# Kernel optimization log

Hardware: AMD Instinct MI355X
Metric: run time of the kernel (lower is better)

## Reference

```python
import jax, jax.numpy as jnp
import numpy as np

NUM_HEADS = 8
HEAD_SIZE = 64
INPUT = 512
OUT = NUM_HEADS * HEAD_SIZE
B, S = 4, 2048


def setup_inputs() -> dict:
    key = jax.random.key(0)
    ks = jax.random.split(key, 6)
    return {
        "key": jax.random.normal(ks[0], (B, S, INPUT), dtype=jnp.float32),
        "key_mask": jnp.zeros((B, 1, 1, S), dtype=jnp.float32),
        "query": jax.random.normal(ks[1], (B, S, INPUT), dtype=jnp.float32),
        "value": jax.random.normal(ks[2], (B, S, INPUT), dtype=jnp.float32),
        "wq": jax.random.normal(ks[3], (INPUT, OUT), dtype=jnp.float32) * (INPUT ** -0.5),
        "wk": jax.random.normal(ks[4], (INPUT, OUT), dtype=jnp.float32) * (INPUT ** -0.5),
        "wv": jax.random.normal(ks[5], (INPUT, OUT), dtype=jnp.float32) * (INPUT ** -0.5),
    }


def _split_heads(x):
    # [B, S, H*hd] -> [B, H, S, hd]
    b, s, _ = x.shape
    return x.reshape(b, s, NUM_HEADS, HEAD_SIZE).transpose(0, 2, 1, 3)


def reference(key, key_mask, query, value, wq, wk, wv):
    q = _split_heads(query @ wq)   # [B,H,S,hd]
    k = _split_heads(key @ wk)
    v = _split_heads(value @ wv)
    scale = 1.0 / jnp.sqrt(jnp.asarray(HEAD_SIZE, q.dtype))
    logits = jnp.einsum('bhqd,bhkd->bhqk', q, k) * scale + key_mask
    attn = jax.nn.softmax(logits, axis=-1)
    out = jnp.einsum('bhqk,bhkd->bhqd', attn, v)  # [B,H,S,hd]
    out = out.transpose(0, 2, 1, 3).reshape(out.shape[0], out.shape[2], OUT)
    return out
```

## Files before the change

kernel.cpp:

```cpp
#include <hip/hip_runtime.h>

typedef _Float16 f16;
typedef f16 f16x8 __attribute__((ext_vector_type(8)));
typedef f16 f16x4 __attribute__((ext_vector_type(4)));
typedef f16 f16x2 __attribute__((ext_vector_type(2)));
typedef float f32x4 __attribute__((ext_vector_type(4)));
typedef unsigned int u32;

#define MFMA16(a, b, c) __builtin_amdgcn_mfma_f32_16x16x32_f16(a, b, c, 0, 0, 0)

#define BATCH 4
#define NHEADS 8
#define HDIM 64
#define SEQ 2048
#define DIN 512
#define DOUT 512
#define LOG2E 1.44269504f
#define C1 0.18033688f

__device__ __forceinline__ void gl_lds16(const void* g, const void* l) {
  __builtin_amdgcn_global_load_lds(
      (const __attribute__((address_space(1))) u32*)g,
      (__attribute__((address_space(3))) u32*)l, 16, 0, 0);
}

__device__ __forceinline__ float fexp2(float x) {
  float r;
  asm("v_exp_f32 %0, %1" : "=v"(r) : "v"(x));
  return r;
}

__device__ __forceinline__ f16x2 pk2(float a, float b) {
  return __builtin_bit_cast(f16x2, __builtin_amdgcn_cvt_pkrtz(a, b));
}

__device__ __forceinline__ f16x4 pk4(float a, float b, float c, float d) {
  f16x2 u0 = pk2(a, b), u1 = pk2(c, d);
  f16x4 r;
  r[0] = u0[0]; r[1] = u0[1]; r[2] = u1[0]; r[3] = u1[1];
  return r;
}

__global__ __launch_bounds__(256) void prep_w(
    const float* __restrict__ wq, const float* __restrict__ wk,
    const float* __restrict__ wv, f16* __restrict__ wT) {
  __shared__ float tile[64][65];
  const float* w = blockIdx.z == 0 ? wq : (blockIdx.z == 1 ? wk : wv);
  f16* out = wT + (size_t)blockIdx.z * DIN * DOUT;
  int k0 = blockIdx.x * 64, n0 = blockIdx.y * 64;
  int t = threadIdx.x;
  int c = t & 63, rb = t >> 6;
#pragma unroll
  for (int ph = 0; ph < 16; ++ph) {
    int r = ph * 4 + rb;
    tile[r][c] = w[(size_t)(k0 + r) * DOUT + n0 + c];
  }
  __syncthreads();
#pragma unroll
  for (int ph = 0; ph < 16; ++ph) {
    int n = ph * 4 + rb;
    out[(size_t)(n0 + n) * DIN + k0 + c] = (f16)tile[c][n];
  }
}

__global__ __launch_bounds__(256, 3) void qkv_gemm(
    const float* __restrict__ xq, const float* __restrict__ xk,
    const float* __restrict__ xv, const f16* __restrict__ wT,
    f16* __restrict__ Qo, f16* __restrict__ Ko, f16* __restrict__ Vt) {
  __shared__ __attribute__((aligned(16))) f16 smem[16384];
  f16* As = smem;
  f16* Bs = smem + 8192;
  f16* CT = smem;

  int gemm = blockIdx.z;
  const float* x = gemm == 0 ? xq : (gemm == 1 ? xk : xv);
  const f16* wt = wT + (size_t)gemm * DIN * DOUT;
  int bx = blockIdx.x;
  int m0 = (bx & 63) * 128, n0 = (bx >> 6) * 128;
  int t = threadIdx.x, w = t >> 6, lane = t & 63;
  int lr = lane & 15, lq = lane >> 4;
  int wm = (w >> 1) * 64, wn = (w & 1) * 64;

  int tr = t >> 4, tc = t & 15;
  const float* xg = x + (size_t)(m0 + tr) * DIN + tc * 4;
  int aw[8];
#pragma unroll
  for (int ph = 0; ph < 8; ++ph) {
    int r = tr + 16 * ph;
    int phys = (tc >> 1) ^ (r & 7);
    aw[ph] = r * 64 + phys * 8 + (tc & 1) * 4;
  }

  int srow = lane >> 3;
  int schunk = (lane & 7) ^ srow;
  const f16* gb[4];
  const f16* lbb[4];
#pragma unroll
  for (int j = 0; j < 4; ++j) {
    int br = w * 32 + j * 8;
    gb[j] = wt + (size_t)(n0 + br + srow) * DIN + schunk * 8;
    lbb[j] = &Bs[__builtin_amdgcn_readfirstlane(br * 64)];
  }
  int xo0 = ((0 * 4 + lq) ^ (lr & 7)) * 8;
  int xo1 = ((1 * 4 + lq) ^ (lr & 7)) * 8;

  f32x4 zero = {0.f, 0.f, 0.f, 0.f};
  f32x4 acc[4][4];
#pragma unroll
  for (int i = 0; i < 4; ++i)
#pragma unroll
    for (int j = 0; j < 4; ++j) acc[i][j] = zero;

  for (int k0 = 0; k0 < DIN; k0 += 64) {
    __syncthreads();
#pragma unroll
    for (int j = 0; j < 4; ++j) gl_lds16(gb[j] + k0, lbb[j]);
#pragma unroll
    for (int ph = 0; ph < 8; ++ph) {
      float4 a = *(const float4*)(xg + (size_t)ph * 16 * DIN + k0);
      *(f16x4*)&As[aw[ph]] = pk4(a.x, a.y, a.z, a.w);
    }
    __syncthreads();
#pragma unroll
    for (int c = 0; c < 2; ++c) {
      int xo = c ? xo1 : xo0;
      f16x8 xf[4], wf[4];
#pragma unroll
      for (int i = 0; i < 4; ++i)
        xf[i] = *(const f16x8*)&As[(wm + i * 16 + lr) * 64 + xo];
#pragma unroll
      for (int i = 0; i < 4; ++i)
        wf[i] = *(const f16x8*)&Bs[(wn + i * 16 + lr) * 64 + xo];
      if (gemm == 2) {
#pragma unroll
        for (int i = 0; i < 4; ++i)
#pragma unroll
          for (int j = 0; j < 4; ++j)
            acc[i][j] = MFMA16(xf[i], wf[j], acc[i][j]);
      } else {
#pragma unroll
        for (int i = 0; i < 4; ++i)
#pragma unroll
          for (int j = 0; j < 4; ++j)
            acc[i][j] = MFMA16(wf[i], xf[j], acc[i][j]);
      }
    }
  }

  __syncthreads();
  int b_ = m0 >> 11;
  int sl = m0 & 2047;

  if (gemm == 2) {
#pragma unroll
    for (int i = 0; i < 4; ++i) {
#pragma unroll
      for (int j = 0; j < 4; ++j) {
        int d = wn + j * 16 + lr;
        int lc = (wm >> 3) + i * 2 + (lq >> 1);
        int phys = lc ^ lr;
        *(f16x4*)&CT[d * 128 + phys * 8 + (lq & 1) * 4] =
            pk4(acc[i][j][0], acc[i][j][1], acc[i][j][2], acc[i][j][3]);
      }
    }
    __syncthreads();
    int tid16 = t & 15;
#pragma unroll
    for (int ph = 0; ph < 8; ++ph) {
      int d = ph * 16 + (t >> 4);
      int phys = tid16 ^ (d & 15);
      f16x8 vv = *(const f16x8*)&CT[d * 128 + phys * 8];
      int hgl = (n0 + d) >> 6, dd = (n0 + d) & 63;
      *(f16x8*)&Vt[(((size_t)b_ * NHEADS + hgl) * HDIM + dd) * SEQ + sl +
                   tid16 * 8] = vv;
    }
  } else {
    f16* O = gemm == 0 ? Qo : Ko;
    float sc = gemm == 0 ? C1 : 1.0f;
#pragma unroll
    for (int i = 0; i < 4; ++i) {
#pragma unroll
      for (int j = 0; j < 4; ++j) {
        int s = wm + j * 16 + lr;
        int lc = (wn >> 3) + i * 2 + (lq >> 1);
        int phys = lc ^ lr;
        *(f16x4*)&CT[s * 128 + phys * 8 + (lq & 1) * 4] =
            pk4(acc[i][j][0] * sc, acc[i][j][1] * sc, acc[i][j][2] * sc,
                acc[i][j][3] * sc);
      }
    }
    __syncthreads();
    int tid8 = t & 7;
    int hh = (t >> 3) & 1;
#pragma unroll
    for (int ph = 0; ph < 8; ++ph) {
      int s = ph * 16 + (t >> 4);
      int lc = hh * 8 + tid8;
      int phys = lc ^ (s & 15);
      f16x8 vv = *(const f16x8*)&CT[s * 128 + phys * 8];
      int hgl = (n0 >> 6) + hh;
      *(f16x8*)&O[(((size_t)b_ * NHEADS + hgl) * SEQ + sl + s) * HDIM +
                  tid8 * 8] = vv;
    }
  }
}

__global__ __launch_bounds__(256, 2) void flash_attn(
    const f16* __restrict__ Q, const f16* __restrict__ K,
    const f16* __restrict__ Vt, const float* __restrict__ mask,
    float* __restrict__ out) {
  __shared__ __attribute__((aligned(16))) f16 Ks[128 * 64];
  __shared__ __attribute__((aligned(16))) f16 Vs[64 * 128];
  __shared__ __attribute__((aligned(16))) f16 Ps[128 * 136];

  int bh = blockIdx.x, q0 = blockIdx.y * 128;
  int b = bh >> 3, h = bh & 7;
  int t = threadIdx.x, w = t >> 6, lane = t & 63;
  int lr = lane & 15, lq = lane >> 4;

  const f16* Qg = Q + (size_t)bh * SEQ * HDIM;
  const f16* Kg = K + (size_t)bh * SEQ * HDIM;
  const f16* Vg = Vt + (size_t)bh * HDIM * SEQ;
  const float* mg = mask + (size_t)b * SEQ;

  f16x8 qf[2][2];
#pragma unroll
  for (int u = 0; u < 2; ++u)
#pragma unroll
    for (int c = 0; c < 2; ++c)
      qf[u][c] = *(const f16x8*)(Qg +
                                 (size_t)(q0 + w * 32 + u * 16 + lr) * HDIM +
                                 c * 32 + lq * 8);

  int krow = lane >> 3;
  int kchunk = (lane & 7) ^ krow;
  const f16* gk[4];
  const f16* gv[4];
  const f16* lk[4];
  const f16* lv[4];
#pragma unroll
  for (int j = 0; j < 4; ++j) {
    int kbr = w * 32 + j * 8;
    gk[j] = Kg + (size_t)(kbr + krow) * HDIM + kchunk * 8;
    lk[j] = &Ks[__builtin_amdgcn_readfirstlane(kbr * 64)];
    int vbr = w * 16 + j * 4;
    int vchunk = (lane & 15) ^ (j * 4 + lq);
    gv[j] = Vg + (size_t)(vbr + lq) * SEQ + vchunk * 8;
    lv[j] = &Vs[__builtin_amdgcn_readfirstlane(vbr * 128)];
  }
  int xk0 = ((0 * 4 + lq) ^ (lr & 7)) * 8;
  int xk1 = ((1 * 4 + lq) ^ (lr & 7)) * 8;

  f32x4 zero = {0.f, 0.f, 0.f, 0.f};
  f32x4 acc[2][4];
#pragma unroll
  for (int u = 0; u < 2; ++u)
#pragma unroll
    for (int i = 0; i < 4; ++i) acc[u][i] = zero;
  float lsum[2] = {0.f, 0.f};

  for (int k0 = 0; k0 < SEQ; k0 += 128) {
    __syncthreads();
#pragma unroll
    for (int j = 0; j < 4; ++j) {
      gl_lds16(gk[j] + (size_t)k0 * HDIM, lk[j]);
      gl_lds16(gv[j] + k0, lv[j]);
    }
    __syncthreads();

    f32x4 s[2][8];
#pragma unroll
    for (int nt = 0; nt < 8; ++nt) {
      f16x8 kf0 = *(const f16x8*)&Ks[(nt * 16 + lr) * 64 + xk0];
      f16x8 kf1 = *(const f16x8*)&Ks[(nt * 16 + lr) * 64 + xk1];
      s[0][nt] = MFMA16(kf0, qf[0][0], zero);
      s[0][nt] = MFMA16(kf1, qf[0][1], s[0][nt]);
      s[1][nt] = MFMA16(kf0, qf[1][0], zero);
      s[1][nt] = MFMA16(kf1, qf[1][1], s[1][nt]);
    }

#pragma unroll
    for (int nt = 0; nt < 8; ++nt) {
      float4 mk = *(const float4*)(mg + k0 + nt * 16 + lq * 4);
#pragma unroll
      for (int u = 0; u < 2; ++u) {
        float p0 = fexp2(fmaf(mk.x, LOG2E, s[u][nt][0]));
        float p1 = fexp2(fmaf(mk.y, LOG2E, s[u][nt][1]));
        float p2 = fexp2(fmaf(mk.z, LOG2E, s[u][nt][2]));
        float p3 = fexp2(fmaf(mk.w, LOG2E, s[u][nt][3]));
        lsum[u] += (p0 + p1) + (p2 + p3);
        *(f16x4*)&Ps[(w * 32 + u * 16 + lr) * 136 + nt * 16 + lq * 4] =
            pk4(p0, p1, p2, p3);
      }
    }

#pragma unroll
    for (int ks = 0; ks < 4; ++ks) {
      f16x8 ap0 = *(const f16x8*)&Ps[(w * 32 + lr) * 136 + ks * 32 + lq * 8];
      f16x8 ap1 =
          *(const f16x8*)&Ps[(w * 32 + 16 + lr) * 136 + ks * 32 + lq * 8];
#pragma unroll
      for (int dt = 0; dt < 4; ++dt) {
        f16x8 bv = *(const f16x8*)&Vs[(dt * 16 + lr) * 128 +
                                      (((ks * 4 + lq) ^ lr) * 8)];
        acc[0][dt] = MFMA16(ap0, bv, acc[0][dt]);
        acc[1][dt] = MFMA16(ap1, bv, acc[1][dt]);
      }
    }
  }

#pragma unroll
  for (int u = 0; u < 2; ++u) {
    float l = lsum[u];
    l += __shfl_xor(l, 16);
    l += __shfl_xor(l, 32);
    float inv = 1.f / l;
    float iv[4];
#pragma unroll
    for (int r = 0; r < 4; ++r) iv[r] = __shfl(inv, lq * 4 + r);
#pragma unroll
    for (int dt = 0; dt < 4; ++dt) {
#pragma unroll
      for (int r = 0; r < 4; ++r) {
        int q = q0 + w * 32 + u * 16 + lq * 4 + r;
        int d = h * HDIM + dt * 16 + lr;
        out[((size_t)b * SEQ + q) * DOUT + d] = acc[u][dt][r] * iv[r];
      }
    }
  }
}

extern "C" void kernel_launch(void* const* d_in, const int* in_sizes, int n_in,
                              void* d_out, int out_size, void* d_ws,
                              size_t ws_size, hipStream_t stream) {
  const float* key = (const float*)d_in[0];
  const float* key_mask = (const float*)d_in[1];
  const float* query = (const float*)d_in[2];
  const float* value = (const float*)d_in[3];
  const float* wq = (const float*)d_in[4];
  const float* wk = (const float*)d_in[5];
  const float* wv = (const float*)d_in[6];
  float* out = (float*)d_out;

  char* ws = (char*)d_ws;
  f16* Qws = (f16*)(ws);
  f16* Kws = (f16*)(ws + 8388608);
  f16* Vtws = (f16*)(ws + 16777216);
  f16* wT = (f16*)(ws + 25165824);

  prep_w<<<dim3(8, 8, 3), 256, 0, stream>>>(wq, wk, wv, wT);
  qkv_gemm<<<dim3(256, 1, 3), 256, 0, stream>>>(query, key, value, wT, Qws,
                                                Kws, Vtws);
  flash_attn<<<dim3(32, 16), 256, 0, stream>>>(Qws, Kws, Vtws, key_mask, out);
}
```

Baseline: 183.8 us.

## Double-buffer K/V tiles with 64-key blocks and raise occupancy to three blocks

The attention loop now processes 64 keys per iteration instead of 128. K and V tiles are double-buffered in LDS, so the next tile's global-to-LDS load is issued before computing on the current one. The P buffer shrinks to a 64-wide XOR-swizzled layout instead of padding, which lowers LDS use enough to request three blocks per CU. This aims to overlap memory latency with MFMA work and raise occupancy. In exchange it adds twice as many loop iterations and barriers, and it relies on a single barrier per iteration to order the buffer reuse and the P writes and reads.

Result: slower. 195.6 us (+6.4%).

```diff
diff --git a/kernel.cpp b/kernel.cpp
--- a/kernel.cpp
+++ b/kernel.cpp
@@ -205,13 +205,13 @@
   }
 }
 
-__global__ __launch_bounds__(256, 2) void flash_attn(
+__global__ __launch_bounds__(256, 3) void flash_attn(
     const f16* __restrict__ Q, const f16* __restrict__ K,
     const f16* __restrict__ Vt, const float* __restrict__ mask,
     float* __restrict__ out) {
-  __shared__ __attribute__((aligned(16))) f16 Ks[128 * 64];
-  __shared__ __attribute__((aligned(16))) f16 Vs[64 * 128];
-  __shared__ __attribute__((aligned(16))) f16 Ps[128 * 136];
+  __shared__ __attribute__((aligned(16))) f16 Ks[2][64 * 64];
+  __shared__ __attribute__((aligned(16))) f16 Vs[2][64 * 64];
+  __shared__ __attribute__((aligned(16))) f16 Ps[128 * 64];
 
   int bh = blockIdx.x, q0 = blockIdx.y * 128;
   int b = bh >> 3, h = bh & 7;
@@ -232,22 +232,11 @@
                                  (size_t)(q0 + w * 32 + u * 16 + lr) * HDIM +
                                  c * 32 + lq * 8);
 
-  int krow = lane >> 3;
-  int kchunk = (lane & 7) ^ krow;
-  const f16* gk[4];
-  const f16* gv[4];
-  const f16* lk[4];
-  const f16* lv[4];
-#pragma unroll
-  for (int j = 0; j < 4; ++j) {
-    int kbr = w * 32 + j * 8;
-    gk[j] = Kg + (size_t)(kbr + krow) * HDIM + kchunk * 8;
-    lk[j] = &Ks[__builtin_amdgcn_readfirstlane(kbr * 64)];
-    int vbr = w * 16 + j * 4;
-    int vchunk = (lane & 15) ^ (j * 4 + lq);
-    gv[j] = Vg + (size_t)(vbr + lq) * SEQ + vchunk * 8;
-    lv[j] = &Vs[__builtin_amdgcn_readfirstlane(vbr * 128)];
-  }
+  int srow = lane >> 3;
+  int sch = (lane & 7) ^ srow;
+  const f16* gk0 = Kg + (size_t)(w * 16 + srow) * HDIM + sch * 8;
+  const f16* gv0 = Vg + (size_t)(w * 16 + srow) * SEQ + sch * 8;
+  int lofs = __builtin_amdgcn_readfirstlane(w * 1024);
   int xk0 = ((0 * 4 + lq) ^ (lr & 7)) * 8;
   int xk1 = ((1 * 4 + lq) ^ (lr & 7)) * 8;
 
@@ -259,20 +248,32 @@
     for (int i = 0; i < 4; ++i) acc[u][i] = zero;
   float lsum[2] = {0.f, 0.f};
 
-  for (int k0 = 0; k0 < SEQ; k0 += 128) {
-    __syncthreads();
-#pragma unroll
-    for (int j = 0; j < 4; ++j) {
-      gl_lds16(gk[j] + (size_t)k0 * HDIM, lk[j]);
-      gl_lds16(gv[j] + k0, lv[j]);
-    }
-    __syncthreads();
-
-    f32x4 s[2][8];
-#pragma unroll
-    for (int nt = 0; nt < 8; ++nt) {
-      f16x8 kf0 = *(const f16x8*)&Ks[(nt * 16 + lr) * 64 + xk0];
-      f16x8 kf1 = *(const f16x8*)&Ks[(nt * 16 + lr) * 64 + xk1];
+#pragma unroll
+  for (int j = 0; j < 2; ++j) {
+    gl_lds16(gk0 + (size_t)j * 8 * HDIM, &Ks[0][lofs + j * 512]);
+    gl_lds16(gv0 + (size_t)j * 8 * SEQ, &Vs[0][lofs + j * 512]);
+  }
+
+  for (int it = 0; it < 32; ++it) {
+    int cur = it & 1;
+    int k0 = it * 64;
+    __syncthreads();
+    if (it < 31) {
+      int k1 = k0 + 64;
+#pragma unroll
+      for (int j = 0; j < 2; ++j) {
+        gl_lds16(gk0 + (size_t)(k1 + j * 8) * HDIM,
+                 &Ks[cur ^ 1][lofs + j * 512]);
+        gl_lds16(gv0 + (size_t)j * 8 * SEQ + k1,
+                 &Vs[cur ^ 1][lofs + j * 512]);
+      }
+    }
+
+    f32x4 s[2][4];
+#pragma unroll
+    for (int nt = 0; nt < 4; ++nt) {
+      f16x8 kf0 = *(const f16x8*)&Ks[cur][(nt * 16 + lr) * 64 + xk0];
+      f16x8 kf1 = *(const f16x8*)&Ks[cur][(nt * 16 + lr) * 64 + xk1];
       s[0][nt] = MFMA16(kf0, qf[0][0], zero);
       s[0][nt] = MFMA16(kf1, qf[0][1], s[0][nt]);
       s[1][nt] = MFMA16(kf0, qf[1][0], zero);
@@ -280,7 +281,7 @@
     }
 
 #pragma unroll
-    for (int nt = 0; nt < 8; ++nt) {
+    for (int nt = 0; nt < 4; ++nt) {
       float4 mk = *(const float4*)(mg + k0 + nt * 16 + lq * 4);
 #pragma unroll
       for (int u = 0; u < 2; ++u) {
@@ -289,20 +290,20 @@
         float p2 = fexp2(fmaf(mk.z, LOG2E, s[u][nt][2]));
         float p3 = fexp2(fmaf(mk.w, LOG2E, s[u][nt][3]));
         lsum[u] += (p0 + p1) + (p2 + p3);
-        *(f16x4*)&Ps[(w * 32 + u * 16 + lr) * 136 + nt * 16 + lq * 4] =
+        int phys = (nt * 2 + (lq >> 1)) ^ (lr & 7);
+        *(f16x4*)&Ps[(w * 32 + u * 16 + lr) * 64 + phys * 8 + (lq & 1) * 4] =
             pk4(p0, p1, p2, p3);
       }
     }
 
 #pragma unroll
-    for (int ks = 0; ks < 4; ++ks) {
-      f16x8 ap0 = *(const f16x8*)&Ps[(w * 32 + lr) * 136 + ks * 32 + lq * 8];
-      f16x8 ap1 =
-          *(const f16x8*)&Ps[(w * 32 + 16 + lr) * 136 + ks * 32 + lq * 8];
+    for (int ks = 0; ks < 2; ++ks) {
+      int pc = ((ks * 4 + lq) ^ (lr & 7)) * 8;
+      f16x8 ap0 = *(const f16x8*)&Ps[(w * 32 + lr) * 64 + pc];
+      f16x8 ap1 = *(const f16x8*)&Ps[(w * 32 + 16 + lr) * 64 + pc];
 #pragma unroll
       for (int dt = 0; dt < 4; ++dt) {
-        f16x8 bv = *(const f16x8*)&Vs[(dt * 16 + lr) * 128 +
-                                      (((ks * 4 + lq) ^ lr) * 8)];
+        f16x8 bv = *(const f16x8*)&Vs[cur][(dt * 16 + lr) * 64 + pc];
         acc[0][dt] = MFMA16(ap0, bv, acc[0][dt]);
         acc[1][dt] = MFMA16(ap1, bv, acc[1][dt]);
       }
```
